# Kernel optimization log

Hardware: AMD Instinct MI355X
Metric: run time of the kernel (lower is better)

## Reference

```python
import jax, jax.numpy as jnp
import numpy as np

B, L, CIN = 32768, 35, 21
N_FLANK, C_FLANK, PEP_MAX = 10, 10, 15
F, K, H = 128, 9, 64


def setup_inputs() -> dict:
    key = jax.random.key(0)
    ks = jax.random.split(key, 16)
    s = lambda k, shape, scale=0.05: jax.random.normal(k, shape, dtype=jnp.float32) * scale
    return {
        "sequence": jax.random.normal(ks[0], (B, L, CIN), dtype=jnp.float32),
        "peptide_length": jax.random.randint(ks[1], (B,), 5, PEP_MAX + 1, dtype=jnp.int32),
        # main conv, weight in WIO layout (k, in, out)
        "conv_w": s(ks[2], (K, CIN, F)),
        "conv_b": jnp.zeros((F,), jnp.float32),
        # n-flank post 1x1 convs (as matmuls)
        "n_w1": s(ks[3], (F, H)), "n_b1": jnp.zeros((H,), jnp.float32),
        "n_w2": s(ks[4], (H, 1)), "n_b2": jnp.zeros((1,), jnp.float32),
        # c-flank post 1x1 convs
        "c_w1": s(ks[5], (F, H)), "c_b1": jnp.zeros((H,), jnp.float32),
        "c_w2": s(ks[6], (H, 1)), "c_b2": jnp.zeros((1,), jnp.float32),
        # flank-average dense layers
        "navg_w": s(ks[7], (F, 1)), "navg_b": jnp.zeros((1,), jnp.float32),
        "cavg_w": s(ks[8], (F, 1)), "cavg_b": jnp.zeros((1,), jnp.float32),
        # output layer: init ones / zeros as in the torch module
        "out_w": jnp.ones((6, 1), jnp.float32),
        "out_b": jnp.zeros((1,), jnp.float32),
    }


def _post(x, w1, b1, w2, b2):
    # stack of 1x1 convs: relu on hidden, tanh on final single-output layer
    h = jax.nn.relu(jnp.einsum("blf,fh->blh", x, w1) + b1)
    return jnp.tanh(jnp.einsum("blh,ho->blo", h, w2) + b2)  # [B, L, 1]


def _masked_neg_max(y, mask):
    # torch: max over dim1 of (y+1)*mask, minus 1, negated
    m = mask[..., None].astype(y.dtype)
    return -(jnp.max((y + 1.0) * m, axis=1) - 1.0)  # [B, 1]


def reference(sequence, peptide_length, conv_w, conv_b, n_w1, n_b1, n_w2, n_b2,
              c_w1, c_b1, c_w2, c_b2, navg_w, navg_b, cavg_w, cavg_b, out_w, out_b):
    # main conv, padding='same', relu activation (dropout rate 0 -> no-op)
    x = jax.lax.conv_general_dilated(
        sequence, conv_w, window_strides=(1,), padding="SAME",
        dimension_numbers=("NWC", "WIO", "NWC"))
    conv_result = jax.nn.relu(x + conv_b)  # [B, L, F]

    plen = peptide_length.reshape(-1)
    pos = jnp.arange(L)[None, :]  # [1, L]

    # --- n-flank branch ---
    yn = _post(conv_result, n_w1, n_b1, n_w2, n_b2)  # [B, L, 1]
    cleaved_n = yn[:, N_FLANK, :]  # [B, 1]
    mask_n = (pos >= N_FLANK + 1) & (pos < (N_FLANK + plen)[:, None])
    maxpool_n = _masked_neg_max(yn, mask_n)
    avg_n = jnp.tanh(jnp.mean(conv_result[:, :N_FLANK], axis=1) @ navg_w + navg_b)

    # --- c-flank branch ---
    yc = _post(conv_result, c_w1, c_b1, c_w2, c_b2)  # [B, L, 1]
    c_idx = (N_FLANK + plen - 1).astype(jnp.int32)
    cleaved_c = jnp.take_along_axis(yc, c_idx[:, None, None], axis=1)[:, 0, :]  # [B, 1]
    mask_c = (pos >= N_FLANK) & (pos < (N_FLANK + plen - 1)[:, None])
    maxpool_c = _masked_neg_max(yc, mask_c)
    starts = (N_FLANK + plen)[:, None]
    mask_cf = ((pos >= starts) & (pos < starts + C_FLANK))[..., None].astype(conv_result.dtype)
    s = jnp.sum((conv_result + 1.0) * mask_cf, axis=1)  # [B, F]
    cnt = jnp.clip(jnp.sum(mask_cf, axis=1), 1.0, None)
    avg_c = jnp.tanh((s / cnt - 1.0) @ cavg_w + cavg_b)

    combined = jnp.concatenate(
        [cleaved_n, maxpool_n, avg_n, cleaved_c, maxpool_c, avg_c], axis=-1)  # [B, 6]
    out = jax.nn.sigmoid(combined @ out_w + out_b)
    return out[:, 0]  # [B]
```

## Files before the change

### kernel.cpp

```cpp
#include <hip/hip_runtime.h>
#include <hip/hip_bf16.h>
#include <math.h>

#define Ln     35
#define CINn   21
#define CINP   24
#define Fn     128
#define Kn     9
#define Hn     64
#define GB     16
#define SEQ_STRIDE 1064
#define TILE_STRIDE 136
#define YP_STRIDE 136

typedef __attribute__((ext_vector_type(8))) short short8;
typedef __attribute__((ext_vector_type(4))) float f32x4;

static __device__ __forceinline__ unsigned short bf16bits(float f) {
    __hip_bfloat16 h = __float2bfloat16(f);
    return *(unsigned short*)&h;
}

template <int CTRL>
static __device__ __forceinline__ float dpp_add(float v) {
    int r = __builtin_amdgcn_update_dpp(0, __builtin_bit_cast(int, v),
                                        CTRL, 0xF, 0xF, true);
    return v + __builtin_bit_cast(float, r);
}
static __device__ __forceinline__ float row_sum16(float v) {
    v = dpp_add<0x128>(v);
    v = dpp_add<0x124>(v);
    v = dpp_add<0x122>(v);
    v = dpp_add<0x121>(v);
    return v;
}

__global__ __launch_bounds__(512, 4) void fused_kernel(
    const float* __restrict__ seq,    const int*   __restrict__ plen_arr,
    const float* __restrict__ conv_w, const float* __restrict__ conv_b,
    const float* __restrict__ n_w1,   const float* __restrict__ n_b1,
    const float* __restrict__ n_w2,   const float* __restrict__ n_b2,
    const float* __restrict__ c_w1,   const float* __restrict__ c_b1,
    const float* __restrict__ c_w2,   const float* __restrict__ c_b2,
    const float* __restrict__ navg_w, const float* __restrict__ navg_b,
    const float* __restrict__ cavg_w, const float* __restrict__ cavg_b,
    const float* __restrict__ out_w,  const float* __restrict__ out_b,
    float* __restrict__ out)
{
    __shared__ __align__(16) unsigned short s_seq[GB * SEQ_STRIDE];
    __shared__ __align__(16) unsigned short s_tile[4][GB * TILE_STRIDE];
    __shared__ __align__(16) float s_yp[Ln * YP_STRIDE];
    float* s_y   = (float*)s_seq;
    float* s_avg = (float*)s_seq + 1152;

    const int t    = threadIdx.x;
    const int wave = t >> 6;
    const int lane = t & 63;
    const int quad = lane >> 4;
    const int col  = lane & 15;
    const int b0   = blockIdx.x * GB;

    {
        uint4* p = (uint4*)s_seq;
        for (int i = t; i < (GB * SEQ_STRIDE) / 8; i += 512)
            p[i] = make_uint4(0u, 0u, 0u, 0u);
    }

    short8 wb[7];
    short8 w1b[4];
    float  cbias[4], b1v, w2v;
    const int head = wave >> 2;
    {
        const int ng = wave * 16 + col;
        #pragma unroll
        for (int s = 0; s < 7; s++) {
            short8 v;
            #pragma unroll
            for (int j = 0; j < 8; j++) {
                int kk = 32 * s + quad * 8 + j;
                int k = kk / CINP, c = kk % CINP;
                float f = (k < Kn && c < CINn) ? conv_w[(k * CINn + c) * Fn + ng] : 0.0f;
                v[j] = (short)bf16bits(f);
            }
            wb[s] = v;
        }
        const int nl = ng & 63;
        #pragma unroll
        for (int s = 0; s < 4; s++) {
            short8 v;
            #pragma unroll
            for (int j = 0; j < 8; j++) {
                int k = 32 * s + quad * 8 + j;
                float f = head ? c_w1[k * Hn + nl] : n_w1[k * Hn + nl];
                v[j] = (short)bf16bits(f);
            }
            w1b[s] = v;
        }
        #pragma unroll
        for (int r = 0; r < 4; r++)
            cbias[r] = conv_b[wave * 16 + 4 * quad + r];
        b1v = head ? c_b1[nl] : n_b1[nl];
        w2v = head ? c_w2[nl] : n_w2[nl];
    }
    const int plen_lane = plen_arr[b0 + col];

    __syncthreads();

    for (int i = t; i < GB * Ln * CINn; i += 512) {
        int bi = i / (Ln * CINn), r = i % (Ln * CINn);
        int l = r / CINn, c = r % CINn;
        s_seq[bi * SEQ_STRIDE + (4 + l) * CINP + c] =
            bf16bits(seq[(size_t)(b0 + bi) * (Ln * CINn) + r]);
    }
    __syncthreads();

    float sum_n[4] = {0.f,0.f,0.f,0.f};
    float sum_c[4] = {0.f,0.f,0.f,0.f};

    for (int l0 = 0; l0 < 36; l0 += 2) {
        const int l1 = l0 + 1;
        short8 af0[7], af1[7];
        #pragma unroll
        for (int s = 0; s < 7; s++) {
            af0[s] = *(const short8*)&s_seq[col * SEQ_STRIDE + l0 * CINP + 32 * s + quad * 8];
            af1[s] = *(const short8*)&s_seq[col * SEQ_STRIDE + l1 * CINP + 32 * s + quad * 8];
        }
        f32x4 cacc0 = {0.f,0.f,0.f,0.f};
        f32x4 cacc1 = {0.f,0.f,0.f,0.f};
        #pragma unroll
        for (int s = 0; s < 7; s++) {
            cacc0 = __builtin_amdgcn_mfma_f32_16x16x32_bf16(wb[s], af0[s], cacc0, 0, 0, 0);
            cacc1 = __builtin_amdgcn_mfma_f32_16x16x32_bf16(wb[s], af1[s], cacc1, 0, 0, 0);
        }
        float a0 = fmaxf(cacc0[0] + cbias[0], 0.0f);
        float a1 = fmaxf(cacc0[1] + cbias[1], 0.0f);
        float a2 = fmaxf(cacc0[2] + cbias[2], 0.0f);
        float a3 = fmaxf(cacc0[3] + cbias[3], 0.0f);
        float e0 = fmaxf(cacc1[0] + cbias[0], 0.0f);
        float e1 = fmaxf(cacc1[1] + cbias[1], 0.0f);
        float e2 = fmaxf(cacc1[2] + cbias[2], 0.0f);
        float e3 = fmaxf(cacc1[3] + cbias[3], 0.0f);
        {
            float cm0 = (l0 >= 10 + plen_lane && l0 < 20 + plen_lane) ? 1.0f : 0.0f;
            float cm1 = (l1 >= 10 + plen_lane && l1 < 20 + plen_lane) ? 1.0f : 0.0f;
            if (l0 < 10) {
                sum_n[0] += a0; sum_n[1] += a1; sum_n[2] += a2; sum_n[3] += a3;
            }
            if (l1 < 10) {
                sum_n[0] += e0; sum_n[1] += e1; sum_n[2] += e2; sum_n[3] += e3;
            }
            sum_c[0] += cm0 * a0 + cm1 * e0;
            sum_c[1] += cm0 * a1 + cm1 * e1;
            sum_c[2] += cm0 * a2 + cm1 * e2;
            sum_c[3] += cm0 * a3 + cm1 * e3;
        }

        if (l0 >= 10 && l0 < 26) {
            ushort4 pk0 = { bf16bits(a0), bf16bits(a1), bf16bits(a2), bf16bits(a3) };
            ushort4 pk1 = { bf16bits(e0), bf16bits(e1), bf16bits(e2), bf16bits(e3) };
            *(ushort4*)&s_tile[l0 & 3][col * TILE_STRIDE + wave * 16 + 4 * quad] = pk0;
            *(ushort4*)&s_tile[l1 & 3][col * TILE_STRIDE + wave * 16 + 4 * quad] = pk1;
            __syncthreads();

            short8 am0[4], am1[4];
            #pragma unroll
            for (int s = 0; s < 4; s++) {
                am0[s] = *(const short8*)&s_tile[l0 & 3][col * TILE_STRIDE + 32 * s + quad * 8];
                am1[s] = *(const short8*)&s_tile[l1 & 3][col * TILE_STRIDE + 32 * s + quad * 8];
            }
            f32x4 hacc0 = {0.f,0.f,0.f,0.f};
            f32x4 hacc1 = {0.f,0.f,0.f,0.f};
            #pragma unroll
            for (int s = 0; s < 4; s++) {
                hacc0 = __builtin_amdgcn_mfma_f32_16x16x32_bf16(am0[s], w1b[s], hacc0, 0, 0, 0);
                hacc1 = __builtin_amdgcn_mfma_f32_16x16x32_bf16(am1[s], w1b[s], hacc1, 0, 0, 0);
            }
            float p0[4], p1[4];
            #pragma unroll
            for (int r = 0; r < 4; r++) {
                p0[r] = row_sum16(fmaxf(hacc0[r] + b1v, 0.f) * w2v);
                p1[r] = row_sum16(fmaxf(hacc1[r] + b1v, 0.f) * w2v);
            }
            if (col == 0) {
                *(f32x4*)&s_yp[l0 * YP_STRIDE + wave * 16 + quad * 4] =
                    (f32x4){p0[0], p0[1], p0[2], p0[3]};
                *(f32x4*)&s_yp[l1 * YP_STRIDE + wave * 16 + quad * 4] =
                    (f32x4){p1[0], p1[1], p1[2], p1[3]};
            }
        }
    }
    __syncthreads();

    {
        float an = 0.f, ac = 0.f;
        #pragma unroll
        for (int r = 0; r < 4; r++) {
            int fidx = wave * 16 + 4 * quad + r;
            an += sum_n[r] * navg_w[fidx];
            ac += sum_c[r] * cavg_w[fidx];
        }
        an += __shfl_xor(an, 16); an += __shfl_xor(an, 32);
        ac += __shfl_xor(ac, 16); ac += __shfl_xor(ac, 32);
        if (quad == 0) {
            s_avg[wave * 2 * GB + 0 * GB + col] = an;
            s_avg[wave * 2 * GB + 1 * GB + col] = ac;
        }
    }
    __syncthreads();

    {
        const float bn = n_b2[0], bc = c_b2[0];
        for (int i = t; i < 2 * GB * 16; i += 512) {
            int m = i & 15, rem = i >> 4;
            int l = 10 + (rem & 15), hd = rem >> 4;
            float v = (hd ? bc : bn);
            #pragma unroll
            for (int w = 0; w < 4; w++)
                v += s_yp[l * YP_STRIDE + (hd * 4 + w) * 16 + m];
            s_y[hd * GB * 36 + m * 36 + l] = tanhf(v);
        }
    }
    __syncthreads();

    if (t < GB) {
        const int m = t;
        const int plen = plen_arr[b0 + m];
        const float* ym = s_y + m * 36;
        const float* yc = s_y + GB * 36 + m * 36;
        float cleaved_n = ym[10];
        float mn = 0.f;
        for (int l = 11; l < 10 + plen; l++) mn = fmaxf(mn, ym[l] + 1.f);
        float maxpool_n = -(mn - 1.f);
        float cleaved_c = yc[10 + plen - 1];
        float mc = 0.f;
        for (int l = 10; l < 10 + plen - 1; l++) mc = fmaxf(mc, yc[l] + 1.f);
        float maxpool_c = -(mc - 1.f);
        float sn = 0.f, sc = 0.f;
        #pragma unroll
        for (int w = 0; w < 8; w++) {
            sn += s_avg[w * 2 * GB + 0 * GB + m];
            sc += s_avg[w * 2 * GB + 1 * GB + m];
        }
        float avg_n = tanhf(sn * 0.1f + navg_b[0]);
        float avg_c = tanhf(sc * 0.1f + cavg_b[0]);
        float comb = cleaved_n * out_w[0] + maxpool_n * out_w[1] + avg_n * out_w[2]
                   + cleaved_c * out_w[3] + maxpool_c * out_w[4] + avg_c * out_w[5]
                   + out_b[0];
        out[b0 + m] = 1.f / (1.f + expf(-comb));
    }
}

extern "C" void kernel_launch(void* const* d_in, const int* in_sizes, int n_in,
                              void* d_out, int out_size, void* d_ws, size_t ws_size,
                              hipStream_t stream) {
    const int B = in_sizes[1];
    fused_kernel<<<B / GB, 512, 0, stream>>>(
        (const float*)d_in[0],  (const int*)d_in[1],
        (const float*)d_in[2],  (const float*)d_in[3],
        (const float*)d_in[4],  (const float*)d_in[5],
        (const float*)d_in[6],  (const float*)d_in[7],
        (const float*)d_in[8],  (const float*)d_in[9],
        (const float*)d_in[10], (const float*)d_in[11],
        (const float*)d_in[12], (const float*)d_in[13],
        (const float*)d_in[14], (const float*)d_in[15],
        (const float*)d_in[16], (const float*)d_in[17],
        (float*)d_out);
}
```

Before: 321.1 us.

## Shrink LDS footprint and vectorize sequence staging loads with float4

Cuts the tile buffer from four slots to two and the partial-score buffer to the 16 positions actually used, which lowers LDS use per block and may let more blocks stay resident. The tile slots are now reused, so a second barrier per position pair is added to protect them. Sequence staging now reads float4 from global memory and scatters the four bf16 values into the padded layout with index adjustments. The extra barrier adds sync cost inside the main loop.

```diff
diff --git a/kernel.cpp b/kernel.cpp
--- a/kernel.cpp
+++ b/kernel.cpp
@@ -12,6 +12,7 @@
 #define SEQ_STRIDE 1064
 #define TILE_STRIDE 136
 #define YP_STRIDE 136
+#define NYL    16
 
 typedef __attribute__((ext_vector_type(8))) short short8;
 typedef __attribute__((ext_vector_type(4))) float f32x4;
@@ -48,8 +49,8 @@
     float* __restrict__ out)
 {
     __shared__ __align__(16) unsigned short s_seq[GB * SEQ_STRIDE];
-    __shared__ __align__(16) unsigned short s_tile[4][GB * TILE_STRIDE];
-    __shared__ __align__(16) float s_yp[Ln * YP_STRIDE];
+    __shared__ __align__(16) unsigned short s_tile[2][GB * TILE_STRIDE];
+    __shared__ __align__(16) float s_yp[NYL * YP_STRIDE];
     float* s_y   = (float*)s_seq;
     float* s_avg = (float*)s_seq + 1152;
 
@@ -106,11 +107,21 @@
 
     __syncthreads();
 
-    for (int i = t; i < GB * Ln * CINn; i += 512) {
-        int bi = i / (Ln * CINn), r = i % (Ln * CINn);
-        int l = r / CINn, c = r % CINn;
-        s_seq[bi * SEQ_STRIDE + (4 + l) * CINP + c] =
-            bf16bits(seq[(size_t)(b0 + bi) * (Ln * CINn) + r]);
+    {
+        const float4* gsrc = (const float4*)(seq + (size_t)b0 * (Ln * CINn));
+        for (int i = t; i < (GB * Ln * CINn) / 4; i += 512) {
+            int i4 = i * 4;
+            int bi = i4 / (Ln * CINn), r = i4 - bi * (Ln * CINn);
+            int l = r / CINn, c = r - l * CINn;
+            float4 v = gsrc[i];
+            int base = bi * SEQ_STRIDE + (4 + l) * CINP + c;
+            #pragma unroll
+            for (int j = 0; j < 4; j++) {
+                float fj = (j == 0) ? v.x : (j == 1) ? v.y : (j == 2) ? v.z : v.w;
+                int adj = ((c + j >= CINn) ? 3 : 0) + ((r + j >= Ln * CINn) ? 224 : 0);
+                s_seq[base + j + adj] = bf16bits(fj);
+            }
+        }
     }
     __syncthreads();
 
@@ -158,15 +169,15 @@
         if (l0 >= 10 && l0 < 26) {
             ushort4 pk0 = { bf16bits(a0), bf16bits(a1), bf16bits(a2), bf16bits(a3) };
             ushort4 pk1 = { bf16bits(e0), bf16bits(e1), bf16bits(e2), bf16bits(e3) };
-            *(ushort4*)&s_tile[l0 & 3][col * TILE_STRIDE + wave * 16 + 4 * quad] = pk0;
-            *(ushort4*)&s_tile[l1 & 3][col * TILE_STRIDE + wave * 16 + 4 * quad] = pk1;
+            *(ushort4*)&s_tile[0][col * TILE_STRIDE + wave * 16 + 4 * quad] = pk0;
+            *(ushort4*)&s_tile[1][col * TILE_STRIDE + wave * 16 + 4 * quad] = pk1;
             __syncthreads();
 
             short8 am0[4], am1[4];
             #pragma unroll
             for (int s = 0; s < 4; s++) {
-                am0[s] = *(const short8*)&s_tile[l0 & 3][col * TILE_STRIDE + 32 * s + quad * 8];
-                am1[s] = *(const short8*)&s_tile[l1 & 3][col * TILE_STRIDE + 32 * s + quad * 8];
+                am0[s] = *(const short8*)&s_tile[0][col * TILE_STRIDE + 32 * s + quad * 8];
+                am1[s] = *(const short8*)&s_tile[1][col * TILE_STRIDE + 32 * s + quad * 8];
             }
             f32x4 hacc0 = {0.f,0.f,0.f,0.f};
             f32x4 hacc1 = {0.f,0.f,0.f,0.f};
@@ -182,11 +193,12 @@
                 p1[r] = row_sum16(fmaxf(hacc1[r] + b1v, 0.f) * w2v);
             }
             if (col == 0) {
-                *(f32x4*)&s_yp[l0 * YP_STRIDE + wave * 16 + quad * 4] =
+                *(f32x4*)&s_yp[(l0 - 10) * YP_STRIDE + wave * 16 + quad * 4] =
                     (f32x4){p0[0], p0[1], p0[2], p0[3]};
-                *(f32x4*)&s_yp[l1 * YP_STRIDE + wave * 16 + quad * 4] =
+                *(f32x4*)&s_yp[(l1 - 10) * YP_STRIDE + wave * 16 + quad * 4] =
                     (f32x4){p1[0], p1[1], p1[2], p1[3]};
             }
+            __syncthreads();
         }
     }
     __syncthreads();
@@ -210,14 +222,14 @@
 
     {
         const float bn = n_b2[0], bc = c_b2[0];
-        for (int i = t; i < 2 * GB * 16; i += 512) {
+        for (int i = t; i < 2 * GB * NYL; i += 512) {
             int m = i & 15, rem = i >> 4;
-            int l = 10 + (rem & 15), hd = rem >> 4;
+            int li = rem & 15, hd = rem >> 4;
             float v = (hd ? bc : bn);
             #pragma unroll
             for (int w = 0; w < 4; w++)
-                v += s_yp[l * YP_STRIDE + (hd * 4 + w) * 16 + m];
-            s_y[hd * GB * 36 + m * 36 + l] = tanhf(v);
+                v += s_yp[li * YP_STRIDE + (hd * 4 + w) * 16 + m];
+            s_y[hd * GB * 36 + m * 36 + (10 + li)] = tanhf(v);
         }
     }
     __syncthreads();
```

Measured after the change: 308.8 us. -3.8%, faster.
